# Optimization experiments

Measured on AMD Instinct MI355X. Metric: run time of the kernel, lower is better.

Reference implementation:

```python
import jax, jax.numpy as jnp
import numpy as np

B, L, IN_DIM, D_MODEL = 4, 1024, 128, 256
MDIM = 2 * D_MODEL          # mamba_dim = 512 (must equal 2*d_model for shape consistency)
NL = 4                      # mamba_layers
DIN = 2 * MDIM              # d_inner (expand=2)
NST = 16                    # d_state
DTR = MDIM // 16            # dt_rank = 32
KC = 4                      # d_conv
EPS = 1e-5

# sinusoidal positional encoding buffer (deterministic)
_pos = np.arange(L, dtype=np.float32)[:, None]
_div = np.exp(np.arange(0, MDIM, 2, dtype=np.float32) * (-np.log(10000.0) / MDIM))
_pe = np.zeros((L, MDIM), dtype=np.float32)
_pe[:, 0::2] = np.sin(_pos * _div)
_pe[:, 1::2] = np.cos(_pos * _div)
PE = jnp.asarray(_pe)


def setup_inputs() -> dict:
    key = jax.random.key(0)
    ks = iter(jax.random.split(key, 64))
    rn = lambda shape, s=0.02: jax.random.normal(next(ks), shape, jnp.float32) * s
    inp = {
        "x": jax.random.normal(next(ks), (B, L, IN_DIM), jnp.float32),
        "rtg": jax.random.normal(next(ks), (B, L, 1), jnp.float32),
        "state_emb_w": rn((D_MODEL, IN_DIM)), "state_emb_b": jnp.zeros((D_MODEL,)),
        "reward_emb_w": rn((D_MODEL, 1)), "reward_emb_b": jnp.zeros((D_MODEL,)),
        "ln_w": jnp.ones((MDIM,)), "ln_b": jnp.zeros((MDIM,)),
        "in_proj_w": rn((NL, 2 * DIN, MDIM)),
        "conv_w": rn((NL, DIN, KC), 0.1), "conv_b": jnp.zeros((NL, DIN)),
        "x_proj_w": rn((NL, DTR + 2 * NST, DIN)),
        "dt_proj_w": rn((NL, DIN, DTR), 0.1), "dt_proj_b": jnp.full((NL, DIN), -2.0),
        "A_log": jnp.tile(jnp.log(jnp.arange(1, NST + 1, dtype=jnp.float32)), (NL, DIN, 1)),
        "D_param": jnp.ones((NL, DIN)),
        "out_proj_w": rn((NL, MDIM, DIN)),
        "norm_w": jnp.ones((NL, MDIM)), "norm_f_w": jnp.ones((MDIM,)),
        "so_w1": rn((MDIM // 2, MDIM)), "so_b1": jnp.zeros((MDIM // 2,)),
        "so_w2": rn((IN_DIM, MDIM // 2)), "so_b2": jnp.zeros((IN_DIM,)),
        "ro_w1": rn((MDIM // 2, MDIM)), "ro_b1": jnp.zeros((MDIM // 2,)),
        "ro_w2": rn((1, MDIM // 2)), "ro_b2": jnp.zeros((1,)),
    }
    return inp


def _rmsnorm(h, w):
    return h * jax.lax.rsqrt(jnp.mean(h * h, -1, keepdims=True) + EPS) * w


def _mamba(h, ipw, cw, cb, xpw, dpw, dpb, Alog, Dp, opw):
    # h: [B,L,MDIM]
    Ls = h.shape[1]
    xz = h @ ipw.T                                   # [B,L,2*DIN]
    xx, z = jnp.split(xz, 2, axis=-1)
    # causal depthwise conv, kernel KC, left pad KC-1
    xp = jnp.pad(xx, ((0, 0), (KC - 1, 0), (0, 0)))
    xc = cb + sum(cw[:, k] * xp[:, k:k + Ls, :] for k in range(KC))
    xc = jax.nn.silu(xc)                             # [B,L,DIN]
    dbc = xc @ xpw.T                                 # [B,L,DTR+2*NST]
    dt = jax.nn.softplus(dbc[..., :DTR] @ dpw.T + dpb)   # [B,L,DIN]
    Bm = dbc[..., DTR:DTR + NST]                     # [B,L,NST]
    Cm = dbc[..., DTR + NST:]                        # [B,L,NST]
    A = -jnp.exp(Alog)                               # [DIN,NST]

    def step(hc, inp):
        dt_t, B_t, C_t, x_t = inp                    # [B,DIN],[B,NST],[B,NST],[B,DIN]
        hc = jnp.exp(dt_t[:, :, None] * A) * hc + (dt_t * x_t)[:, :, None] * B_t[:, None, :]
        return hc, jnp.einsum('bdn,bn->bd', hc, C_t)

    h0 = jnp.zeros((h.shape[0], DIN, NST), h.dtype)
    _, ys = jax.lax.scan(step, h0, (dt.swapaxes(0, 1), Bm.swapaxes(0, 1),
                                    Cm.swapaxes(0, 1), xc.swapaxes(0, 1)))
    y = ys.swapaxes(0, 1) + Dp * xc
    y = y * jax.nn.silu(z)
    return y @ opw.T                                 # [B,L,MDIM]


def _forward(x, rtg, state_emb_w, state_emb_b, reward_emb_w, reward_emb_b, ln_w, ln_b,
             in_proj_w, conv_w, conv_b, x_proj_w, dt_proj_w, dt_proj_b, A_log, D_param,
             out_proj_w, norm_w, norm_f_w, so_w1, so_b1, so_w2, so_b2, ro_w1, ro_b1, ro_w2, ro_b2):
    se = x @ state_emb_w.T + state_emb_b            # [B,L,D_MODEL]
    re = rtg @ reward_emb_w.T + reward_emb_b        # [B,L,D_MODEL]
    h = jnp.concatenate([se, re], axis=-1)          # [B,L,MDIM]
    h = h + PE[:h.shape[1]]                          # dropout is identity at eval
    mu = jnp.mean(h, -1, keepdims=True)
    var = jnp.var(h, -1, keepdims=True)
    h = (h - mu) * jax.lax.rsqrt(var + EPS) * ln_w + ln_b
    residual = None
    for i in range(NL):
        residual = h if residual is None else h + residual
        hn = _rmsnorm(residual, norm_w[i])
        h = _mamba(hn, in_proj_w[i], conv_w[i], conv_b[i], x_proj_w[i],
                   dt_proj_w[i], dt_proj_b[i], A_log[i], D_param[i], out_proj_w[i])
    residual = h + residual
    h = _rmsnorm(residual, norm_f_w)
    next_state = jax.nn.relu(h @ so_w1.T + so_b1) @ so_w2.T + so_b2   # [B,L,IN_DIM]
    next_reward = jax.nn.relu(h @ ro_w1.T + ro_b1) @ ro_w2.T + ro_b2  # [B,L,1]
    return next_state, next_reward


def reference(x, rtg, state_emb_w, state_emb_b, reward_emb_w, reward_emb_b, ln_w, ln_b,
              in_proj_w, conv_w, conv_b, x_proj_w, dt_proj_w, dt_proj_b, A_log, D_param,
              out_proj_w, norm_w, norm_f_w, so_w1, so_b1, so_w2, so_b2, ro_w1, ro_b1, ro_w2, ro_b2):
    return _forward(x, rtg, state_emb_w, state_emb_b, reward_emb_w, reward_emb_b, ln_w, ln_b,
                    in_proj_w, conv_w, conv_b, x_proj_w, dt_proj_w, dt_proj_b, A_log, D_param,
                    out_proj_w, norm_w, norm_f_w, so_w1, so_b1, so_w2, so_b2, ro_w1, ro_b1, ro_w2, ro_b2)
```

## Files before the change

kernel.cpp:

```cpp
#include <hip/hip_runtime.h>
#include <stdint.h>

typedef unsigned short u16;
typedef __attribute__((ext_vector_type(8))) short bf16x8;
typedef __attribute__((ext_vector_type(8))) u16 u16x8;
typedef __attribute__((ext_vector_type(4))) float f32x4;

static __device__ __forceinline__ u16 f2b(float f) {
  uint32_t u = __builtin_bit_cast(uint32_t, f);
  u += 0x7fffu + ((u >> 16) & 1u);
  return (u16)(u >> 16);
}
static __device__ __forceinline__ float b2f(u16 h) {
  uint32_t u = ((uint32_t)h) << 16;
  return __builtin_bit_cast(float, u);
}

#define GLDS16(gsrc, ldst)                                                        \
  __builtin_amdgcn_global_load_lds(                                               \
      (const __attribute__((address_space(1))) void*)(gsrc),                      \
      (__attribute__((address_space(3))) void*)(ldst), 16, 0, 0)

__global__ __launch_bounds__(256) void cvt6_kernel(
    const float* __restrict__ a0, u16* __restrict__ b0,
    const float* __restrict__ a1, u16* __restrict__ b1,
    const float* __restrict__ a2, u16* __restrict__ b2,
    const float* __restrict__ a3, u16* __restrict__ b3,
    const float* __restrict__ a4, u16* __restrict__ b4,
    const float* __restrict__ a5, u16* __restrict__ b5) {
  int i = blockIdx.x * 256 + threadIdx.x;
  const int n0 = 4194304, n1 = 262144, n2 = 2097152, n3 = 131072, n4 = 32768, n5 = 131072;
  if (i < n0) { b0[i] = f2b(a0[i]); return; } i -= n0;
  if (i < n1) { b1[i] = f2b(a1[i]); return; } i -= n1;
  if (i < n2) { b2[i] = f2b(a2[i]); return; } i -= n2;
  if (i < n3) { b3[i] = f2b(a3[i]); return; } i -= n3;
  if (i < n4) { b4[i] = f2b(a4[i]); return; } i -= n4;
  if (i < n5) { b5[i] = f2b(a5[i]); }
}

__global__ __launch_bounds__(256) void pe_kernel(float* __restrict__ PEt) {
  const int l = blockIdx.x;
  const float c = -9.210340371976184f / 512.f;
#pragma unroll
  for (int q = 0; q < 2; ++q) {
    int dd = threadIdx.x + q * 256;
    float div = expf((float)(2 * (dd >> 1)) * c);
    float v = (dd & 1) ? cosf((float)l * div) : sinf((float)l * div);
    PEt[(size_t)l * 512 + dd] = v;
  }
}

__global__ __launch_bounds__(256) void dpw_t_kernel(const float* __restrict__ dpw,
                                                    float* __restrict__ dpwT) {
  const int l = blockIdx.y;
  int idx = blockIdx.x * 256 + threadIdx.x;
  int j = idx >> 10, dd = idx & 1023;
  dpwT[(size_t)l * 32768 + idx] = dpw[(size_t)l * 32768 + (size_t)dd * 32 + j];
}

__global__ __launch_bounds__(256) void embed_ln2(
    const float* __restrict__ x, const float* __restrict__ rtg,
    const float* __restrict__ Wse, const float* __restrict__ bse,
    const float* __restrict__ Wre, const float* __restrict__ bre,
    const float* __restrict__ lnw, const float* __restrict__ lnb,
    const float* __restrict__ PEt, float* __restrict__ h) {
  const int tid = threadIdx.x;
  const int tok0 = blockIdx.x * 16;
  const int l0 = tok0 & 1023;
  __shared__ float xs[16][128];
  __shared__ float rt[16];
  __shared__ float sw[16][2][4];
  for (int i = tid; i < 16 * 128; i += 256) ((float*)xs)[i] = x[(size_t)tok0 * 128 + i];
  if (tid < 16) rt[tid] = rtg[tok0 + tid];
  __syncthreads();
  const int d = tid;
  float acc[16];
#pragma unroll
  for (int tt = 0; tt < 16; ++tt) acc[tt] = 0.f;
  const float* wrow = Wse + (size_t)d * 128;
  for (int k0 = 0; k0 < 128; k0 += 8) {
    float4 wa = *(const float4*)(wrow + k0);
    float4 wb = *(const float4*)(wrow + k0 + 4);
#pragma unroll
    for (int tt = 0; tt < 16; ++tt) {
      const float* xr = &xs[tt][k0];
      acc[tt] += xr[0] * wa.x + xr[1] * wa.y + xr[2] * wa.z + xr[3] * wa.w +
                 xr[4] * wb.x + xr[5] * wb.y + xr[6] * wb.z + xr[7] * wb.w;
    }
  }
  const float seb = bse[d], reW = Wre[d], reB = bre[d];
  const int lane = tid & 63, wv = tid >> 6;
  float h1a[16];
#pragma unroll
  for (int tt = 0; tt < 16; ++tt) {
    float h0 = acc[tt] + seb + PEt[(size_t)(l0 + tt) * 512 + d];
    float h1 = reB + rt[tt] * reW + PEt[(size_t)(l0 + tt) * 512 + 256 + d];
    acc[tt] = h0;
    h1a[tt] = h1;
    float s = h0 + h1, q = h0 * h0 + h1 * h1;
#pragma unroll
    for (int o = 32; o; o >>= 1) { s += __shfl_xor(s, o); q += __shfl_xor(q, o); }
    if (lane == 0) { sw[tt][0][wv] = s; sw[tt][1][wv] = q; }
  }
  __syncthreads();
#pragma unroll
  for (int tt = 0; tt < 16; ++tt) {
    float S = sw[tt][0][0] + sw[tt][0][1] + sw[tt][0][2] + sw[tt][0][3];
    float Q = sw[tt][1][0] + sw[tt][1][1] + sw[tt][1][2] + sw[tt][1][3];
    float mean = S * (1.f / 512.f);
    float var = Q * (1.f / 512.f) - mean * mean;
    float rstd = rsqrtf(var + 1e-5f);
    size_t base = (size_t)(tok0 + tt) * 512;
    h[base + d]       = (acc[tt] - mean) * rstd * lnw[d] + lnb[d];
    h[base + 256 + d] = (h1a[tt] - mean) * rstd * lnw[256 + d] + lnb[256 + d];
  }
}

__global__ __launch_bounds__(256) void resid_rms_kernel(
    const float* __restrict__ hin, float* __restrict__ residual,
    const float* __restrict__ w, u16* __restrict__ outb, int first) {
  const int tok = blockIdx.x;
  const int t = threadIdx.x;
  __shared__ float rq[4];
  size_t base = (size_t)tok * 512;
  float v0 = hin[base + t], v1 = hin[base + t + 256];
  if (!first) { v0 += residual[base + t]; v1 += residual[base + t + 256]; }
  residual[base + t] = v0;
  residual[base + t + 256] = v1;
  float q = v0 * v0 + v1 * v1;
#pragma unroll
  for (int o = 32; o; o >>= 1) q += __shfl_xor(q, o);
  if ((t & 63) == 0) rq[t >> 6] = q;
  __syncthreads();
  float Q = rq[0] + rq[1] + rq[2] + rq[3];
  float scale = rsqrtf(Q * (1.f / 512.f) + 1e-5f);
  outb[base + t]       = f2b(v0 * scale * w[t]);
  outb[base + t + 256] = f2b(v1 * scale * w[t + 256]);
}

template <int BM, int BN, int WM, int WN, int EPI>
__global__ __launch_bounds__(256) void gemm_bt(
    const u16* __restrict__ A, const u16* __restrict__ Bw,
    float* __restrict__ Cf, u16* __restrict__ Cb,
    const float* __restrict__ bias, int M, int N, int K) {
  constexpr int MF = BM / (WM * 16);
  constexpr int NF = BN / (WN * 16);
  constexpr int NCA = (BM * 4) / 256;
  constexpr int NCB = (BN * 4) / 256;
  __shared__ __align__(16) u16 lA[BM * 32];
  __shared__ __align__(16) u16 lB[BN * 32];
  const int tid = threadIdx.x;
  const int lane = tid & 63;
  const int wv = tid >> 6;
  const int wr = wv / WN, wc = wv % WN;
  const int m0 = blockIdx.x * BM, n0 = blockIdx.y * BN;
  const int kchunk = K / gridDim.z;
  const int kb = blockIdx.z * kchunk;

  f32x4 acc[MF][NF];
#pragma unroll
  for (int i = 0; i < MF; ++i)
#pragma unroll
    for (int j = 0; j < NF; ++j) acc[i][j] = (f32x4){0.f, 0.f, 0.f, 0.f};

  const int srow = tid >> 2, sck = tid & 3;
  const u16* Ag = A + (size_t)(m0 + srow) * K + sck * 8 + kb;
  const u16* Bg = Bw + (size_t)(n0 + srow) * K + sck * 8 + kb;

  for (int k0 = 0; k0 < kchunk; k0 += 32) {
#pragma unroll
    for (int it = 0; it < NCA; ++it)
      GLDS16(Ag + (size_t)it * 64 * K + k0, &lA[(it * 256 + tid) * 8]);
#pragma unroll
    for (int it = 0; it < NCB; ++it)
      GLDS16(Bg + (size_t)it * 64 * K + k0, &lB[(it * 256 + tid) * 8]);
    __syncthreads();
    bf16x8 af[MF], bfr[NF];
    const int koff = (lane >> 4) * 8;
#pragma unroll
    for (int mi = 0; mi < MF; ++mi) {
      int r = wr * (MF * 16) + mi * 16 + (lane & 15);
      af[mi] = *(const bf16x8*)(&lA[r * 32 + koff]);
    }
#pragma unroll
    for (int ni = 0; ni < NF; ++ni) {
      int r = wc * (NF * 16) + ni * 16 + (lane & 15);
      bfr[ni] = *(const bf16x8*)(&lB[r * 32 + koff]);
    }
#pragma unroll
    for (int mi = 0; mi < MF; ++mi)
#pragma unroll
      for (int ni = 0; ni < NF; ++ni)
        acc[mi][ni] = __builtin_amdgcn_mfma_f32_16x16x32_bf16(af[mi], bfr[ni], acc[mi][ni], 0, 0, 0);
    __syncthreads();
  }

  float* co = Cf + (size_t)blockIdx.z * (size_t)M * N;
  const int rbase = (lane >> 4) * 4;
  const int cbase = lane & 15;
#pragma unroll
  for (int mi = 0; mi < MF; ++mi) {
#pragma unroll
    for (int ni = 0; ni < NF; ++ni) {
      int row = m0 + wr * (MF * 16) + mi * 16 + rbase;
      int col = n0 + wc * (NF * 16) + ni * 16 + cbase;
      float bv = (EPI >= 2) ? bias[col] : 0.f;
#pragma unroll
      for (int r = 0; r < 4; ++r) {
        float v = acc[mi][ni][r] + bv;
        if (EPI == 2) v = fmaxf(v, 0.f);
        size_t idx = (size_t)(row + r) * N + col;
        if (EPI == 1 || EPI == 2) Cb[idx] = f2b(v);
        else co[idx] = v;
      }
    }
  }
}

__global__ __launch_bounds__(256) void conv_silu_kernel2(
    const u16* __restrict__ xz, const float* __restrict__ cw,
    const float* __restrict__ cb, u16* __restrict__ xcb) {
  int gid = blockIdx.x * 256 + threadIdx.x;
  int d0 = (gid & 127) * 8;
  int token = gid >> 7;
  int t = token & 1023;
  const u16* xx = xz + (size_t)(token - t) * 2048 + d0;
  float s[8];
#pragma unroll
  for (int j = 0; j < 8; ++j) s[j] = cb[d0 + j];
#pragma unroll
  for (int k = 0; k < 4; ++k) {
    int tt = t - 3 + k;
    if (tt >= 0) {
      u16x8 v = *(const u16x8*)(xx + (size_t)tt * 2048);
#pragma unroll
      for (int j = 0; j < 8; ++j) s[j] += cw[(size_t)(d0 + j) * 4 + k] * b2f(v[j]);
    }
  }
  u16x8 o;
#pragma unroll
  for (int j = 0; j < 8; ++j) {
    float sl = s[j] / (1.f + expf(-s[j]));
    o[j] = f2b(sl);
  }
  *(u16x8*)(xcb + (size_t)token * 1024 + d0) = o;
}

__global__ __launch_bounds__(256) void dt_kernel2(
    const float* __restrict__ P, const float* __restrict__ dpwT,
    const float* __restrict__ dpb, u16* __restrict__ dtout,
    float* __restrict__ dbcr) {
  const int tid = threadIdx.x;
  const int tok0 = blockIdx.x * 16;
  __shared__ float sm[16][64];
  const size_t str = (size_t)4096 * 64;
  for (int i = tid; i < 16 * 64; i += 256) {
    size_t o = (size_t)tok0 * 64 + i;
    float v = P[o] + P[str + o] + P[2 * str + o] + P[3 * str + o];
    ((float*)sm)[i] = v;
    dbcr[o] = v;
  }
  __syncthreads();
  float acc0[16], acc1[16], acc2[16], acc3[16];
#pragma unroll
  for (int t = 0; t < 16; ++t) { acc0[t] = 0.f; acc1[t] = 0.f; acc2[t] = 0.f; acc3[t] = 0.f; }
#pragma unroll 4
  for (int j = 0; j < 32; ++j) {
    float w0 = dpwT[(size_t)j * 1024 + tid];
    float w1 = dpwT[(size_t)j * 1024 + 256 + tid];
    float w2 = dpwT[(size_t)j * 1024 + 512 + tid];
    float w3 = dpwT[(size_t)j * 1024 + 768 + tid];
#pragma unroll
    for (int t = 0; t < 16; ++t) {
      float sv = sm[t][j];
      acc0[t] += sv * w0;
      acc1[t] += sv * w1;
      acc2[t] += sv * w2;
      acc3[t] += sv * w3;
    }
  }
  const float b0 = dpb[tid], b1 = dpb[256 + tid], b2 = dpb[512 + tid], b3 = dpb[768 + tid];
#pragma unroll
  for (int t = 0; t < 16; ++t) {
    size_t o = (size_t)(tok0 + t) * 1024 + tid;
    float a0 = acc0[t] + b0, a1 = acc1[t] + b1, a2 = acc2[t] + b2, a3 = acc3[t] + b3;
    dtout[o]       = f2b((a0 > 20.f) ? a0 : logf(1.f + expf(a0)));
    dtout[o + 256] = f2b((a1 > 20.f) ? a1 : logf(1.f + expf(a1)));
    dtout[o + 512] = f2b((a2 > 20.f) ? a2 : logf(1.f + expf(a2)));
    dtout[o + 768] = f2b((a3 > 20.f) ? a3 : logf(1.f + expf(a3)));
  }
}

__global__ __launch_bounds__(256) void scan1(
    const u16* __restrict__ dt, const u16* __restrict__ xc,
    const float* __restrict__ dbc, const float* __restrict__ Alog,
    float* __restrict__ Ubuf, float* __restrict__ SD, int NCc, int TCc) {
  const int d = blockIdx.x * 256 + threadIdx.x;
  const int c = blockIdx.y;
  const int b = blockIdx.z;
  const int t0 = c * TCc;
  __shared__ __align__(16) float sB[64][16];
  for (int i = threadIdx.x; i < TCc * 16; i += 256) {
    int t = i >> 4, n = i & 15;
    sB[t][n] = dbc[((size_t)(b * 1024 + t0 + t)) * 64 + 32 + n];
  }
  float A2[16];
#pragma unroll
  for (int q = 0; q < 4; ++q) {
    float4 a4 = *(const float4*)(Alog + (size_t)d * 16 + q * 4);
    A2[q * 4 + 0] = -expf(a4.x) * 1.4426950408889634f;
    A2[q * 4 + 1] = -expf(a4.y) * 1.4426950408889634f;
    A2[q * 4 + 2] = -expf(a4.z) * 1.4426950408889634f;
    A2[q * 4 + 3] = -expf(a4.w) * 1.4426950408889634f;
  }
  __syncthreads();
  float hc[16];
#pragma unroll
  for (int n = 0; n < 16; ++n) hc[n] = 0.f;
  float sumdt = 0.f;
  size_t tok = (size_t)b * 1024 + t0;
  for (int t = 0; t < TCc; ++t, ++tok) {
    float dtv = b2f(dt[tok * 1024 + d]);
    float xcv = b2f(xc[tok * 1024 + d]);
    float du = dtv * xcv;
    sumdt += dtv;
#pragma unroll
    for (int q = 0; q < 4; ++q) {
      float4 B4 = *(const float4*)(&sB[t][q * 4]);
      float e0 = exp2f(dtv * A2[q * 4 + 0]);
      float e1 = exp2f(dtv * A2[q * 4 + 1]);
      float e2 = exp2f(dtv * A2[q * 4 + 2]);
      float e3 = exp2f(dtv * A2[q * 4 + 3]);
      hc[q * 4 + 0] = e0 * hc[q * 4 + 0] + du * B4.x;
      hc[q * 4 + 1] = e1 * hc[q * 4 + 1] + du * B4.y;
      hc[q * 4 + 2] = e2 * hc[q * 4 + 2] + du * B4.z;
      hc[q * 4 + 3] = e3 * hc[q * 4 + 3] + du * B4.w;
    }
  }
  size_t ob = (((size_t)b * NCc + c) * 16) * 1024 + d;
#pragma unroll
  for (int n = 0; n < 16; ++n) Ubuf[ob + (size_t)n * 1024] = hc[n];
  SD[((size_t)b * NCc + c) * 1024 + d] = sumdt;
}

__global__ __launch_bounds__(256) void scan_mid(
    const float* __restrict__ Ubuf, const float* __restrict__ SD,
    const float* __restrict__ Alog, float* __restrict__ H0, int NCc) {
  int idx = blockIdx.x * 256 + threadIdx.x;
  int b = idx >> 14;
  int nd = idx & 16383;
  int n = nd >> 10, d = nd & 1023;
  const float A2 = -expf(Alog[(size_t)d * 16 + n]) * 1.4426950408889634f;
  float h = 0.f;
  size_t o0 = ((size_t)b * NCc * 16) * 1024 + nd;
  const size_t cstr = (size_t)16 * 1024;
  size_t sd0 = ((size_t)b * NCc) * 1024 + d;
  for (int cc = 0; cc < NCc; ++cc) {
    size_t o = o0 + (size_t)cc * cstr;
    H0[o] = h;
    if (cc < NCc - 1) {
      float e = exp2f(A2 * SD[sd0 + (size_t)cc * 1024]);
      h = e * h + Ubuf[o];
    }
  }
}

__global__ __launch_bounds__(256) void scan2(
    const u16* __restrict__ dt, const u16* __restrict__ xc,
    const float* __restrict__ dbc, const u16* __restrict__ xz,
    const float* __restrict__ Alog, const float* __restrict__ Dp,
    const float* __restrict__ H0, u16* __restrict__ yg, int NCc, int TCc) {
  const int d = blockIdx.x * 256 + threadIdx.x;
  const int c = blockIdx.y;
  const int b = blockIdx.z;
  const int t0 = c * TCc;
  __shared__ __align__(16) float sB[64][16];
  __shared__ __align__(16) float sC[64][16];
  for (int i = threadIdx.x; i < TCc * 16; i += 256) {
    int t = i >> 4, n = i & 15;
    size_t o = ((size_t)(b * 1024 + t0 + t)) * 64 + 32;
    sB[t][n] = dbc[o + n];
    sC[t][n] = dbc[o + 16 + n];
  }
  float A2[16];
#pragma unroll
  for (int q = 0; q < 4; ++q) {
    float4 a4 = *(const float4*)(Alog + (size_t)d * 16 + q * 4);
    A2[q * 4 + 0] = -expf(a4.x) * 1.4426950408889634f;
    A2[q * 4 + 1] = -expf(a4.y) * 1.4426950408889634f;
    A2[q * 4 + 2] = -expf(a4.z) * 1.4426950408889634f;
    A2[q * 4 + 3] = -expf(a4.w) * 1.4426950408889634f;
  }
  const float Dd = Dp[d];
  float hc[16];
  size_t ob = (((size_t)b * NCc + c) * 16) * 1024 + d;
#pragma unroll
  for (int n = 0; n < 16; ++n) hc[n] = H0[ob + (size_t)n * 1024];
  __syncthreads();
  size_t tok = (size_t)b * 1024 + t0;
  for (int t = 0; t < TCc; ++t, ++tok) {
    float dtv = b2f(dt[tok * 1024 + d]);
    float xcv = b2f(xc[tok * 1024 + d]);
    float du = dtv * xcv;
    float y0 = 0.f, y1 = 0.f, y2 = 0.f, y3 = 0.f;
#pragma unroll
    for (int q = 0; q < 4; ++q) {
      float4 B4 = *(const float4*)(&sB[t][q * 4]);
      float4 C4 = *(const float4*)(&sC[t][q * 4]);
      float e0 = exp2f(dtv * A2[q * 4 + 0]);
      float e1 = exp2f(dtv * A2[q * 4 + 1]);
      float e2 = exp2f(dtv * A2[q * 4 + 2]);
      float e3 = exp2f(dtv * A2[q * 4 + 3]);
      hc[q * 4 + 0] = e0 * hc[q * 4 + 0] + du * B4.x;
      hc[q * 4 + 1] = e1 * hc[q * 4 + 1] + du * B4.y;
      hc[q * 4 + 2] = e2 * hc[q * 4 + 2] + du * B4.z;
      hc[q * 4 + 3] = e3 * hc[q * 4 + 3] + du * B4.w;
      y0 += hc[q * 4 + 0] * C4.x;
      y1 += hc[q * 4 + 1] * C4.y;
      y2 += hc[q * 4 + 2] * C4.z;
      y3 += hc[q * 4 + 3] * C4.w;
    }
    float y = (y0 + y1) + (y2 + y3);
    float z = b2f(xz[tok * 2048 + 1024 + d]);
    float g = z / (1.f + expf(-z));
    yg[tok * 1024 + d] = f2b((y + Dd * xcv) * g);
  }
}

__global__ __launch_bounds__(256) void reward_head_kernel(
    const u16* __restrict__ t1r, const float* __restrict__ w2,
    const float* __restrict__ b2, float* __restrict__ outr) {
  int tok = blockIdx.x * 4 + (threadIdx.x >> 6);
  int lane = threadIdx.x & 63;
  float s = 0.f;
#pragma unroll
  for (int j = 0; j < 256; j += 64) s += b2f(t1r[(size_t)tok * 256 + j + lane]) * w2[j + lane];
#pragma unroll
  for (int o = 32; o; o >>= 1) s += __shfl_xor(s, o);
  if (lane == 0) outr[tok] = s + b2[0];
}

extern "C" void kernel_launch(void* const* d_in, const int* in_sizes, int n_in,
                              void* d_out, int out_size, void* d_ws, size_t ws_size,
                              hipStream_t stream) {
  const float* x    = (const float*)d_in[0];
  const float* rtg  = (const float*)d_in[1];
  const float* Wse  = (const float*)d_in[2];
  const float* bse  = (const float*)d_in[3];
  const float* Wre  = (const float*)d_in[4];
  const float* bre  = (const float*)d_in[5];
  const float* lnw  = (const float*)d_in[6];
  const float* lnb  = (const float*)d_in[7];
  const float* ipw  = (const float*)d_in[8];
  const float* cw   = (const float*)d_in[9];
  const float* cb   = (const float*)d_in[10];
  const float* xpw  = (const float*)d_in[11];
  const float* dpw  = (const float*)d_in[12];
  const float* dpb  = (const float*)d_in[13];
  const float* Alog = (const float*)d_in[14];
  const float* Dp   = (const float*)d_in[15];
  const float* opw  = (const float*)d_in[16];
  const float* nw   = (const float*)d_in[17];
  const float* nfw  = (const float*)d_in[18];
  const float* sow1 = (const float*)d_in[19];
  const float* sob1 = (const float*)d_in[20];
  const float* sow2 = (const float*)d_in[21];
  const float* sob2 = (const float*)d_in[22];
  const float* row1 = (const float*)d_in[23];
  const float* rob1 = (const float*)d_in[24];
  const float* row2 = (const float*)d_in[25];
  const float* rob2 = (const float*)d_in[26];
  (void)in_sizes; (void)n_in; (void)out_size;

  char* wsp = (char*)d_ws;
  size_t off = 0;
  auto alloc = [&](size_t bytes) -> void* {
    off = (off + 255) & ~(size_t)255;
    void* p = wsp + off;
    off += bytes;
    return p;
  };
  const int TOK = 4096;
  float* h     = (float*)alloc((size_t)TOK * 512 * 4);
  float* resid = (float*)alloc((size_t)TOK * 512 * 4);
  u16* hn      = (u16*)alloc((size_t)TOK * 512 * 2);
  u16* xzb     = (u16*)alloc((size_t)TOK * 2048 * 2);
  u16* xcb     = (u16*)alloc((size_t)TOK * 1024 * 2);
  float* dbcP  = (float*)alloc((size_t)4 * TOK * 64 * 4);
  float* dbc   = (float*)alloc((size_t)TOK * 64 * 4);
  u16* dtb     = (u16*)alloc((size_t)TOK * 1024 * 2);
  float* PEt   = (float*)alloc((size_t)1024 * 512 * 4);
  float* dpwT  = (float*)alloc((size_t)4 * 32 * 1024 * 4);
  u16* ipwb    = (u16*)alloc((size_t)4 * 2048 * 512 * 2);
  u16* xpwb    = (u16*)alloc((size_t)4 * 64 * 1024 * 2);
  u16* opwb    = (u16*)alloc((size_t)4 * 512 * 1024 * 2);
  u16* sow1b   = (u16*)alloc((size_t)256 * 512 * 2);
  u16* sow2b   = (u16*)alloc((size_t)128 * 256 * 2);
  u16* row1b   = (u16*)alloc((size_t)256 * 512 * 2);

  size_t base_off = (off + 255) & ~(size_t)255;
  auto scan_bytes = [](int nc) {
    return (size_t)2 * 4 * nc * 16 * 1024 * 4 + (size_t)4 * nc * 1024 * 4 + 1024;
  };
  int NCc = 16;
  if (ws_size >= base_off + scan_bytes(64)) NCc = 64;
  else if (ws_size >= base_off + scan_bytes(32)) NCc = 32;
  int TCc = 1024 / NCc;
  char* shared8 = (char*)alloc((size_t)4096 * NCc * 16 * 4);
  float* Ubuf  = (float*)shared8;
  float* H0    = (float*)alloc((size_t)4096 * NCc * 16 * 4);
  float* SD    = (float*)alloc((size_t)4 * NCc * 1024 * 4);
  u16* t1s     = (u16*)shared8;
  u16* t1r     = t1s + (size_t)TOK * 256;

  cvt6_kernel<<<26752, 256, 0, stream>>>(ipw, ipwb, xpw, xpwb, opw, opwb,
                                         sow1, sow1b, sow2, sow2b, row1, row1b);
  pe_kernel<<<1024, 256, 0, stream>>>(PEt);
  dpw_t_kernel<<<dim3(128, 4), 256, 0, stream>>>(dpw, dpwT);
  embed_ln2<<<256, 256, 0, stream>>>(x, rtg, Wse, bse, Wre, bre, lnw, lnb, PEt, h);

  for (int i = 0; i < 4; ++i) {
    resid_rms_kernel<<<TOK, 256, 0, stream>>>(h, resid, nw + i * 512, hn, i == 0);
    gemm_bt<128, 128, 2, 2, 1><<<dim3(32, 16, 1), 256, 0, stream>>>(
        hn, ipwb + (size_t)i * 2048 * 512, nullptr, xzb, nullptr, 4096, 2048, 512);
    conv_silu_kernel2<<<2048, 256, 0, stream>>>(
        xzb, cw + (size_t)i * 4096, cb + i * 1024, xcb);
    gemm_bt<128, 64, 2, 2, 0><<<dim3(32, 1, 4), 256, 0, stream>>>(
        xcb, xpwb + (size_t)i * 64 * 1024, dbcP, nullptr, nullptr, 4096, 64, 1024);
    dt_kernel2<<<TOK / 16, 256, 0, stream>>>(dbcP, dpwT + (size_t)i * 32 * 1024,
                                             dpb + i * 1024, dtb, dbc);
    scan1<<<dim3(4, NCc - 1, 4), 256, 0, stream>>>(
        dtb, xcb, dbc, Alog + (size_t)i * 1024 * 16, Ubuf, SD, NCc, TCc);
    scan_mid<<<256, 256, 0, stream>>>(Ubuf, SD, Alog + (size_t)i * 1024 * 16, H0, NCc);
    scan2<<<dim3(4, NCc, 4), 256, 0, stream>>>(
        dtb, xcb, dbc, xzb, Alog + (size_t)i * 1024 * 16, Dp + i * 1024,
        H0, xcb, NCc, TCc);
    gemm_bt<128, 64, 2, 2, 0><<<dim3(32, 8, 1), 256, 0, stream>>>(
        xcb, opwb + (size_t)i * 512 * 1024, h, nullptr, nullptr, 4096, 512, 1024);
  }

  resid_rms_kernel<<<TOK, 256, 0, stream>>>(h, resid, nfw, hn, 0);
  gemm_bt<64, 64, 2, 2, 2><<<dim3(64, 4, 1), 256, 0, stream>>>(
      hn, sow1b, nullptr, t1s, sob1, 4096, 256, 512);
  gemm_bt<64, 64, 2, 2, 3><<<dim3(64, 2, 1), 256, 0, stream>>>(
      t1s, sow2b, (float*)d_out, nullptr, sob2, 4096, 128, 256);
  gemm_bt<64, 64, 2, 2, 2><<<dim3(64, 4, 1), 256, 0, stream>>>(
      hn, row1b, nullptr, t1r, rob1, 4096, 256, 512);
  reward_head_kernel<<<TOK / 4, 256, 0, stream>>>(
      t1r, row2, rob2, (float*)d_out + (size_t)TOK * 128);
}
```

Before: 776.9 us.

## Fuse scan into one cooperative kernel, merge setup kernels and head GEMMs

```diff
diff --git a/kernel.cpp b/kernel.cpp
--- a/kernel.cpp
+++ b/kernel.cpp
@@ -1,5 +1,8 @@
 #include <hip/hip_runtime.h>
+#include <hip/hip_cooperative_groups.h>
 #include <stdint.h>
+
+namespace cg = cooperative_groups;
 
 typedef unsigned short u16;
 typedef __attribute__((ext_vector_type(8))) short bf16x8;
@@ -21,41 +24,39 @@
       (const __attribute__((address_space(1))) void*)(gsrc),                      \
       (__attribute__((address_space(3))) void*)(ldst), 16, 0, 0)
 
-__global__ __launch_bounds__(256) void cvt6_kernel(
-    const float* __restrict__ a0, u16* __restrict__ b0,
-    const float* __restrict__ a1, u16* __restrict__ b1,
-    const float* __restrict__ a2, u16* __restrict__ b2,
-    const float* __restrict__ a3, u16* __restrict__ b3,
-    const float* __restrict__ a4, u16* __restrict__ b4,
-    const float* __restrict__ a5, u16* __restrict__ b5) {
+__global__ __launch_bounds__(256) void setup_kernel(
+    const float* __restrict__ ipw, u16* __restrict__ ipwb,
+    const float* __restrict__ xpw, u16* __restrict__ xpwb,
+    const float* __restrict__ opw, u16* __restrict__ opwb,
+    const float* __restrict__ sow1, u16* __restrict__ sow1b,
+    const float* __restrict__ sow2, u16* __restrict__ sow2b,
+    const float* __restrict__ row1, u16* __restrict__ row1b,
+    float* __restrict__ PEt,
+    const float* __restrict__ dpw, float* __restrict__ dpwT,
+    const float* __restrict__ cw, float* __restrict__ cwT) {
   int i = blockIdx.x * 256 + threadIdx.x;
-  const int n0 = 4194304, n1 = 262144, n2 = 2097152, n3 = 131072, n4 = 32768, n5 = 131072;
-  if (i < n0) { b0[i] = f2b(a0[i]); return; } i -= n0;
-  if (i < n1) { b1[i] = f2b(a1[i]); return; } i -= n1;
-  if (i < n2) { b2[i] = f2b(a2[i]); return; } i -= n2;
-  if (i < n3) { b3[i] = f2b(a3[i]); return; } i -= n3;
-  if (i < n4) { b4[i] = f2b(a4[i]); return; } i -= n4;
-  if (i < n5) { b5[i] = f2b(a5[i]); }
-}
-
-__global__ __launch_bounds__(256) void pe_kernel(float* __restrict__ PEt) {
-  const int l = blockIdx.x;
-  const float c = -9.210340371976184f / 512.f;
-#pragma unroll
-  for (int q = 0; q < 2; ++q) {
-    int dd = threadIdx.x + q * 256;
-    float div = expf((float)(2 * (dd >> 1)) * c);
-    float v = (dd & 1) ? cosf((float)l * div) : sinf((float)l * div);
-    PEt[(size_t)l * 512 + dd] = v;
-  }
-}
-
-__global__ __launch_bounds__(256) void dpw_t_kernel(const float* __restrict__ dpw,
-                                                    float* __restrict__ dpwT) {
-  const int l = blockIdx.y;
-  int idx = blockIdx.x * 256 + threadIdx.x;
-  int j = idx >> 10, dd = idx & 1023;
-  dpwT[(size_t)l * 32768 + idx] = dpw[(size_t)l * 32768 + (size_t)dd * 32 + j];
+  if (i < 4194304) { ipwb[i] = f2b(ipw[i]); return; } i -= 4194304;
+  if (i < 262144)  { xpwb[i] = f2b(xpw[i]); return; } i -= 262144;
+  if (i < 2097152) { opwb[i] = f2b(opw[i]); return; } i -= 2097152;
+  if (i < 131072)  { sow1b[i] = f2b(sow1[i]); return; } i -= 131072;
+  if (i < 32768)   { sow2b[i] = f2b(sow2[i]); return; } i -= 32768;
+  if (i < 131072)  { row1b[i] = f2b(row1[i]); return; } i -= 131072;
+  if (i < 524288) {
+    int dd = i & 511, l = i >> 9;
+    const float cc = -9.210340371976184f / 512.f;
+    float div = expf((float)(2 * (dd >> 1)) * cc);
+    PEt[i] = (dd & 1) ? cosf((float)l * div) : sinf((float)l * div);
+    return;
+  } i -= 524288;
+  if (i < 131072) {
+    int l = i >> 15, r = i & 32767, j = r >> 10, dd = r & 1023;
+    dpwT[i] = dpw[(size_t)l * 32768 + (size_t)dd * 32 + j];
+    return;
+  } i -= 131072;
+  if (i < 16384) {
+    int l = i >> 12, r = i & 4095, k = r >> 10, dd = r & 1023;
+    cwT[i] = cw[(size_t)l * 4096 + (size_t)dd * 4 + k];
+  }
 }
 
 __global__ __launch_bounds__(256) void embed_ln2(
@@ -142,7 +143,8 @@
 __global__ __launch_bounds__(256) void gemm_bt(
     const u16* __restrict__ A, const u16* __restrict__ Bw,
     float* __restrict__ Cf, u16* __restrict__ Cb,
-    const float* __restrict__ bias, int M, int N, int K) {
+    const float* __restrict__ bias, const float* __restrict__ bias2,
+    int M, int N, int K, int As) {
   constexpr int MF = BM / (WM * 16);
   constexpr int NF = BN / (WN * 16);
   constexpr int NCA = (BM * 4) / 256;
@@ -164,13 +166,13 @@
     for (int j = 0; j < NF; ++j) acc[i][j] = (f32x4){0.f, 0.f, 0.f, 0.f};
 
   const int srow = tid >> 2, sck = tid & 3;
-  const u16* Ag = A + (size_t)(m0 + srow) * K + sck * 8 + kb;
+  const u16* Ag = A + (size_t)(m0 + srow) * As + sck * 8 + kb;
   const u16* Bg = Bw + (size_t)(n0 + srow) * K + sck * 8 + kb;
 
   for (int k0 = 0; k0 < kchunk; k0 += 32) {
 #pragma unroll
     for (int it = 0; it < NCA; ++it)
-      GLDS16(Ag + (size_t)it * 64 * K + k0, &lA[(it * 256 + tid) * 8]);
+      GLDS16(Ag + (size_t)it * 64 * As + k0, &lA[(it * 256 + tid) * 8]);
 #pragma unroll
     for (int it = 0; it < NCB; ++it)
       GLDS16(Bg + (size_t)it * 64 * K + k0, &lB[(it * 256 + tid) * 8]);
@@ -204,21 +206,23 @@
     for (int ni = 0; ni < NF; ++ni) {
       int row = m0 + wr * (MF * 16) + mi * 16 + rbase;
       int col = n0 + wc * (NF * 16) + ni * 16 + cbase;
-      float bv = (EPI >= 2) ? bias[col] : 0.f;
+      float bv = 0.f;
+      if (EPI == 2 || EPI == 3) bv = bias[col];
+      if (EPI == 4) bv = (col < 256) ? bias[col] : bias2[col - 256];
 #pragma unroll
       for (int r = 0; r < 4; ++r) {
         float v = acc[mi][ni][r] + bv;
-        if (EPI == 2) v = fmaxf(v, 0.f);
+        if (EPI == 2 || EPI == 4) v = fmaxf(v, 0.f);
         size_t idx = (size_t)(row + r) * N + col;
-        if (EPI == 1 || EPI == 2) Cb[idx] = f2b(v);
+        if (EPI == 1 || EPI == 2 || EPI == 4) Cb[idx] = f2b(v);
         else co[idx] = v;
       }
     }
   }
 }
 
-__global__ __launch_bounds__(256) void conv_silu_kernel2(
-    const u16* __restrict__ xz, const float* __restrict__ cw,
+__global__ __launch_bounds__(256) void conv_silu3(
+    const u16* __restrict__ xz, const float* __restrict__ cwT,
     const float* __restrict__ cb, u16* __restrict__ xcb) {
   int gid = blockIdx.x * 256 + threadIdx.x;
   int d0 = (gid & 127) * 8;
@@ -226,15 +230,23 @@
   int t = token & 1023;
   const u16* xx = xz + (size_t)(token - t) * 2048 + d0;
   float s[8];
-#pragma unroll
-  for (int j = 0; j < 8; ++j) s[j] = cb[d0 + j];
+  {
+    float4 cba = *(const float4*)(cb + d0);
+    float4 cbb = *(const float4*)(cb + d0 + 4);
+    s[0] = cba.x; s[1] = cba.y; s[2] = cba.z; s[3] = cba.w;
+    s[4] = cbb.x; s[5] = cbb.y; s[6] = cbb.z; s[7] = cbb.w;
+  }
 #pragma unroll
   for (int k = 0; k < 4; ++k) {
     int tt = t - 3 + k;
     if (tt >= 0) {
       u16x8 v = *(const u16x8*)(xx + (size_t)tt * 2048);
-#pragma unroll
-      for (int j = 0; j < 8; ++j) s[j] += cw[(size_t)(d0 + j) * 4 + k] * b2f(v[j]);
+      float4 wA = *(const float4*)(cwT + (size_t)k * 1024 + d0);
+      float4 wB = *(const float4*)(cwT + (size_t)k * 1024 + d0 + 4);
+      s[0] += wA.x * b2f(v[0]); s[1] += wA.y * b2f(v[1]);
+      s[2] += wA.z * b2f(v[2]); s[3] += wA.w * b2f(v[3]);
+      s[4] += wB.x * b2f(v[4]); s[5] += wB.y * b2f(v[5]);
+      s[6] += wB.z * b2f(v[6]); s[7] += wB.w * b2f(v[7]);
     }
   }
   u16x8 o;
@@ -291,18 +303,28 @@
   }
 }
 
-__global__ __launch_bounds__(256) void scan1(
+#define NCF 32
+#define TCF 32
+
+__global__ __launch_bounds__(256, 2) void scanF(
     const u16* __restrict__ dt, const u16* __restrict__ xc,
-    const float* __restrict__ dbc, const float* __restrict__ Alog,
-    float* __restrict__ Ubuf, float* __restrict__ SD, int NCc, int TCc) {
-  const int d = blockIdx.x * 256 + threadIdx.x;
+    const float* __restrict__ dbc, const u16* __restrict__ xz,
+    const float* __restrict__ Alog, const float* __restrict__ Dp,
+    float* __restrict__ Ubuf, float* __restrict__ SD,
+    u16* __restrict__ yg) {
+  const int tid = threadIdx.x;
+  const int d = blockIdx.x * 256 + tid;
   const int c = blockIdx.y;
   const int b = blockIdx.z;
-  const int t0 = c * TCc;
-  __shared__ __align__(16) float sB[64][16];
-  for (int i = threadIdx.x; i < TCc * 16; i += 256) {
+  const int t0 = c * TCF;
+  __shared__ __align__(16) float sB[TCF][16];
+  __shared__ __align__(16) float sC[TCF][16];
+  __shared__ float sYL[TCF][256];
+  for (int i = tid; i < TCF * 16; i += 256) {
     int t = i >> 4, n = i & 15;
-    sB[t][n] = dbc[((size_t)(b * 1024 + t0 + t)) * 64 + 32 + n];
+    size_t o = ((size_t)(b * 1024 + t0 + t)) * 64 + 32;
+    sB[t][n] = dbc[o + n];
+    sC[t][n] = dbc[o + 16 + n];
   }
   float A2[16];
 #pragma unroll
@@ -313,95 +335,21 @@
     A2[q * 4 + 2] = -expf(a4.z) * 1.4426950408889634f;
     A2[q * 4 + 3] = -expf(a4.w) * 1.4426950408889634f;
   }
+  const float Dd = Dp[d];
   __syncthreads();
   float hc[16];
 #pragma unroll
   for (int n = 0; n < 16; ++n) hc[n] = 0.f;
+  float cd[TCF];
   float sumdt = 0.f;
   size_t tok = (size_t)b * 1024 + t0;
-  for (int t = 0; t < TCc; ++t, ++tok) {
+#pragma unroll
+  for (int t = 0; t < TCF; ++t, ++tok) {
     float dtv = b2f(dt[tok * 1024 + d]);
     float xcv = b2f(xc[tok * 1024 + d]);
     float du = dtv * xcv;
     sumdt += dtv;
-#pragma unroll
-    for (int q = 0; q < 4; ++q) {
-      float4 B4 = *(const float4*)(&sB[t][q * 4]);
-      float e0 = exp2f(dtv * A2[q * 4 + 0]);
-      float e1 = exp2f(dtv * A2[q * 4 + 1]);
-      float e2 = exp2f(dtv * A2[q * 4 + 2]);
-      float e3 = exp2f(dtv * A2[q * 4 + 3]);
-      hc[q * 4 + 0] = e0 * hc[q * 4 + 0] + du * B4.x;
-      hc[q * 4 + 1] = e1 * hc[q * 4 + 1] + du * B4.y;
-      hc[q * 4 + 2] = e2 * hc[q * 4 + 2] + du * B4.z;
-      hc[q * 4 + 3] = e3 * hc[q * 4 + 3] + du * B4.w;
-    }
-  }
-  size_t ob = (((size_t)b * NCc + c) * 16) * 1024 + d;
-#pragma unroll
-  for (int n = 0; n < 16; ++n) Ubuf[ob + (size_t)n * 1024] = hc[n];
-  SD[((size_t)b * NCc + c) * 1024 + d] = sumdt;
-}
-
-__global__ __launch_bounds__(256) void scan_mid(
-    const float* __restrict__ Ubuf, const float* __restrict__ SD,
-    const float* __restrict__ Alog, float* __restrict__ H0, int NCc) {
-  int idx = blockIdx.x * 256 + threadIdx.x;
-  int b = idx >> 14;
-  int nd = idx & 16383;
-  int n = nd >> 10, d = nd & 1023;
-  const float A2 = -expf(Alog[(size_t)d * 16 + n]) * 1.4426950408889634f;
-  float h = 0.f;
-  size_t o0 = ((size_t)b * NCc * 16) * 1024 + nd;
-  const size_t cstr = (size_t)16 * 1024;
-  size_t sd0 = ((size_t)b * NCc) * 1024 + d;
-  for (int cc = 0; cc < NCc; ++cc) {
-    size_t o = o0 + (size_t)cc * cstr;
-    H0[o] = h;
-    if (cc < NCc - 1) {
-      float e = exp2f(A2 * SD[sd0 + (size_t)cc * 1024]);
-      h = e * h + Ubuf[o];
-    }
-  }
-}
-
-__global__ __launch_bounds__(256) void scan2(
-    const u16* __restrict__ dt, const u16* __restrict__ xc,
-    const float* __restrict__ dbc, const u16* __restrict__ xz,
-    const float* __restrict__ Alog, const float* __restrict__ Dp,
-    const float* __restrict__ H0, u16* __restrict__ yg, int NCc, int TCc) {
-  const int d = blockIdx.x * 256 + threadIdx.x;
-  const int c = blockIdx.y;
-  const int b = blockIdx.z;
-  const int t0 = c * TCc;
-  __shared__ __align__(16) float sB[64][16];
-  __shared__ __align__(16) float sC[64][16];
-  for (int i = threadIdx.x; i < TCc * 16; i += 256) {
-    int t = i >> 4, n = i & 15;
-    size_t o = ((size_t)(b * 1024 + t0 + t)) * 64 + 32;
-    sB[t][n] = dbc[o + n];
-    sC[t][n] = dbc[o + 16 + n];
-  }
-  float A2[16];
-#pragma unroll
-  for (int q = 0; q < 4; ++q) {
-    float4 a4 = *(const float4*)(Alog + (size_t)d * 16 + q * 4);
-    A2[q * 4 + 0] = -expf(a4.x) * 1.4426950408889634f;
-    A2[q * 4 + 1] = -expf(a4.y) * 1.4426950408889634f;
-    A2[q * 4 + 2] = -expf(a4.z) * 1.4426950408889634f;
-    A2[q * 4 + 3] = -expf(a4.w) * 1.4426950408889634f;
-  }
-  const float Dd = Dp[d];
-  float hc[16];
-  size_t ob = (((size_t)b * NCc + c) * 16) * 1024 + d;
-#pragma unroll
-  for (int n = 0; n < 16; ++n) hc[n] = H0[ob + (size_t)n * 1024];
-  __syncthreads();
-  size_t tok = (size_t)b * 1024 + t0;
-  for (int t = 0; t < TCc; ++t, ++tok) {
-    float dtv = b2f(dt[tok * 1024 + d]);
-    float xcv = b2f(xc[tok * 1024 + d]);
-    float du = dtv * xcv;
+    cd[t] = sumdt;
     float y0 = 0.f, y1 = 0.f, y2 = 0.f, y3 = 0.f;
 #pragma unroll
     for (int q = 0; q < 4; ++q) {
@@ -420,21 +368,63 @@
       y2 += hc[q * 4 + 2] * C4.z;
       y3 += hc[q * 4 + 3] * C4.w;
     }
-    float y = (y0 + y1) + (y2 + y3);
+    sYL[t][tid] = (y0 + y1) + (y2 + y3) + Dd * xcv;
+  }
+  size_t ob = (((size_t)b * NCF + c) * 16) * 1024 + d;
+#pragma unroll
+  for (int n = 0; n < 16; ++n) Ubuf[ob + (size_t)n * 1024] = hc[n];
+  SD[((size_t)b * NCF + c) * 1024 + d] = sumdt;
+
+  cg::this_grid().sync();
+
+  tok = (size_t)b * 1024 + t0;
+  if (c == 0) {
+#pragma unroll
+    for (int t = 0; t < TCF; ++t, ++tok) {
+      float acc = sYL[t][tid];
+      float z = b2f(xz[tok * 2048 + 1024 + d]);
+      float g = z / (1.f + expf(-z));
+      yg[tok * 1024 + d] = f2b(acc * g);
+    }
+    return;
+  }
+  float h0[16];
+#pragma unroll
+  for (int n = 0; n < 16; ++n) h0[n] = 0.f;
+  for (int ccp = 0; ccp < c; ++ccp) {
+    float sd = SD[((size_t)b * NCF + ccp) * 1024 + d];
+    size_t oo = (((size_t)b * NCF + ccp) * 16) * 1024 + d;
+#pragma unroll
+    for (int n = 0; n < 16; ++n)
+      h0[n] = exp2f(A2[n] * sd) * h0[n] + Ubuf[oo + (size_t)n * 1024];
+  }
+#pragma unroll
+  for (int t = 0; t < TCF; ++t, ++tok) {
+    float acc = sYL[t][tid];
+    float cdt = cd[t];
+#pragma unroll
+    for (int q = 0; q < 4; ++q) {
+      float4 C4 = *(const float4*)(&sC[t][q * 4]);
+      acc += C4.x * exp2f(A2[q * 4 + 0] * cdt) * h0[q * 4 + 0];
+      acc += C4.y * exp2f(A2[q * 4 + 1] * cdt) * h0[q * 4 + 1];
+      acc += C4.z * exp2f(A2[q * 4 + 2] * cdt) * h0[q * 4 + 2];
+      acc += C4.w * exp2f(A2[q * 4 + 3] * cdt) * h0[q * 4 + 3];
+    }
     float z = b2f(xz[tok * 2048 + 1024 + d]);
     float g = z / (1.f + expf(-z));
-    yg[tok * 1024 + d] = f2b((y + Dd * xcv) * g);
+    yg[tok * 1024 + d] = f2b(acc * g);
   }
 }
 
 __global__ __launch_bounds__(256) void reward_head_kernel(
-    const u16* __restrict__ t1r, const float* __restrict__ w2,
+    const u16* __restrict__ t1sr, const float* __restrict__ w2,
     const float* __restrict__ b2, float* __restrict__ outr) {
   int tok = blockIdx.x * 4 + (threadIdx.x >> 6);
   int lane = threadIdx.x & 63;
   float s = 0.f;
 #pragma unroll
-  for (int j = 0; j < 256; j += 64) s += b2f(t1r[(size_t)tok * 256 + j + lane]) * w2[j + lane];
+  for (int j = 0; j < 256; j += 64)
+    s += b2f(t1sr[(size_t)tok * 512 + 256 + j + lane]) * w2[j + lane];
 #pragma unroll
   for (int o = 32; o; o >>= 1) s += __shfl_xor(s, o);
   if (lane == 0) outr[tok] = s + b2[0];
@@ -470,7 +460,7 @@
   const float* rob1 = (const float*)d_in[24];
   const float* row2 = (const float*)d_in[25];
   const float* rob2 = (const float*)d_in[26];
-  (void)in_sizes; (void)n_in; (void)out_size;
+  (void)in_sizes; (void)n_in; (void)out_size; (void)ws_size;
 
   char* wsp = (char*)d_ws;
   size_t off = 0;
@@ -491,61 +481,58 @@
   u16* dtb     = (u16*)alloc((size_t)TOK * 1024 * 2);
   float* PEt   = (float*)alloc((size_t)1024 * 512 * 4);
   float* dpwT  = (float*)alloc((size_t)4 * 32 * 1024 * 4);
+  float* cwT   = (float*)alloc((size_t)4 * 4 * 1024 * 4);
   u16* ipwb    = (u16*)alloc((size_t)4 * 2048 * 512 * 2);
   u16* xpwb    = (u16*)alloc((size_t)4 * 64 * 1024 * 2);
   u16* opwb    = (u16*)alloc((size_t)4 * 512 * 1024 * 2);
   u16* sow1b   = (u16*)alloc((size_t)256 * 512 * 2);
+  u16* row1b   = (u16*)alloc((size_t)256 * 512 * 2);
   u16* sow2b   = (u16*)alloc((size_t)128 * 256 * 2);
-  u16* row1b   = (u16*)alloc((size_t)256 * 512 * 2);
-
-  size_t base_off = (off + 255) & ~(size_t)255;
-  auto scan_bytes = [](int nc) {
-    return (size_t)2 * 4 * nc * 16 * 1024 * 4 + (size_t)4 * nc * 1024 * 4 + 1024;
-  };
-  int NCc = 16;
-  if (ws_size >= base_off + scan_bytes(64)) NCc = 64;
-  else if (ws_size >= base_off + scan_bytes(32)) NCc = 32;
-  int TCc = 1024 / NCc;
-  char* shared8 = (char*)alloc((size_t)4096 * NCc * 16 * 4);
-  float* Ubuf  = (float*)shared8;
-  float* H0    = (float*)alloc((size_t)4096 * NCc * 16 * 4);
-  float* SD    = (float*)alloc((size_t)4 * NCc * 1024 * 4);
-  u16* t1s     = (u16*)shared8;
-  u16* t1r     = t1s + (size_t)TOK * 256;
-
-  cvt6_kernel<<<26752, 256, 0, stream>>>(ipw, ipwb, xpw, xpwb, opw, opwb,
-                                         sow1, sow1b, sow2, sow2b, row1, row1b);
-  pe_kernel<<<1024, 256, 0, stream>>>(PEt);
-  dpw_t_kernel<<<dim3(128, 4), 256, 0, stream>>>(dpw, dpwT);
+  float* Ubuf  = (float*)alloc((size_t)4096 * NCF * 16 * 4);
+  float* SD    = (float*)alloc((size_t)4 * NCF * 1024 * 4);
+  u16* t1sr    = (u16*)Ubuf;
+
+  setup_kernel<<<29376, 256, 0, stream>>>(ipw, ipwb, xpw, xpwb, opw, opwb,
+                                          sow1, sow1b, sow2, sow2b, row1, row1b,
+                                          PEt, dpw, dpwT, cw, cwT);
   embed_ln2<<<256, 256, 0, stream>>>(x, rtg, Wse, bse, Wre, bre, lnw, lnb, PEt, h);
 
   for (int i = 0; i < 4; ++i) {
     resid_rms_kernel<<<TOK, 256, 0, stream>>>(h, resid, nw + i * 512, hn, i == 0);
     gemm_bt<128, 128, 2, 2, 1><<<dim3(32, 16, 1), 256, 0, stream>>>(
-        hn, ipwb + (size_t)i * 2048 * 512, nullptr, xzb, nullptr, 4096, 2048, 512);
-    conv_silu_kernel2<<<2048, 256, 0, stream>>>(
-        xzb, cw + (size_t)i * 4096, cb + i * 1024, xcb);
+        hn, ipwb + (size_t)i * 2048 * 512, nullptr, xzb, nullptr, nullptr,
+        4096, 2048, 512, 512);
+    conv_silu3<<<2048, 256, 0, stream>>>(
+        xzb, cwT + (size_t)i * 4096, cb + i * 1024, xcb);
     gemm_bt<128, 64, 2, 2, 0><<<dim3(32, 1, 4), 256, 0, stream>>>(
-        xcb, xpwb + (size_t)i * 64 * 1024, dbcP, nullptr, nullptr, 4096, 64, 1024);
+        xcb, xpwb + (size_t)i * 64 * 1024, dbcP, nullptr, nullptr, nullptr,
+        4096, 64, 1024, 1024);
     dt_kernel2<<<TOK / 16, 256, 0, stream>>>(dbcP, dpwT + (size_t)i * 32 * 1024,
                                              dpb + i * 1024, dtb, dbc);
-    scan1<<<dim3(4, NCc - 1, 4), 256, 0, stream>>>(
-        dtb, xcb, dbc, Alog + (size_t)i * 1024 * 16, Ubuf, SD, NCc, TCc);
-    scan_mid<<<256, 256, 0, stream>>>(Ubuf, SD, Alog + (size_t)i * 1024 * 16, H0, NCc);
-    scan2<<<dim3(4, NCc, 4), 256, 0, stream>>>(
-        dtb, xcb, dbc, xzb, Alog + (size_t)i * 1024 * 16, Dp + i * 1024,
-        H0, xcb, NCc, TCc);
+    {
+      const u16* dtp = dtb;
+      const u16* xcp = xcb;
+      const float* dbcp = dbc;
+      const u16* xzp = xzb;
+      const float* AlogL = Alog + (size_t)i * 1024 * 16;
+      const float* DpL = Dp + (size_t)i * 1024;
+      float* Up = Ubuf;
+      float* SDp = SD;
+      u16* ygp = xcb;
+      void* sargs[] = {&dtp, &xcp, &dbcp, &xzp, &AlogL, &DpL, &Up, &SDp, &ygp};
+      hipLaunchCooperativeKernel((void*)scanF, dim3(4, NCF, 4), dim3(256, 1, 1),
+                                 sargs, 0, stream);
+    }
     gemm_bt<128, 64, 2, 2, 0><<<dim3(32, 8, 1), 256, 0, stream>>>(
-        xcb, opwb + (size_t)i * 512 * 1024, h, nullptr, nullptr, 4096, 512, 1024);
+        xcb, opwb + (size_t)i * 512 * 1024, h, nullptr, nullptr, nullptr,
+        4096, 512, 1024, 1024);
   }
 
   resid_rms_kernel<<<TOK, 256, 0, stream>>>(h, resid, nfw, hn, 0);
-  gemm_bt<64, 64, 2, 2, 2><<<dim3(64, 4, 1), 256, 0, stream>>>(
-      hn, sow1b, nullptr, t1s, sob1, 4096, 256, 512);
+  gemm_bt<64, 64, 2, 2, 4><<<dim3(64, 8, 1), 256, 0, stream>>>(
+      hn, sow1b, nullptr, t1sr, sob1, rob1, 4096, 512, 512, 512);
   gemm_bt<64, 64, 2, 2, 3><<<dim3(64, 2, 1), 256, 0, stream>>>(
-      t1s, sow2b, (float*)d_out, nullptr, sob2, 4096, 128, 256);
-  gemm_bt<64, 64, 2, 2, 2><<<dim3(64, 4, 1), 256, 0, stream>>>(
-      hn, row1b, nullptr, t1r, rob1, 4096, 256, 512);
+      t1sr, sow2b, (float*)d_out, nullptr, sob2, nullptr, 4096, 128, 256, 512);
   reward_head_kernel<<<TOK / 4, 256, 0, stream>>>(
-      t1r, row2, rob2, (float*)d_out + (size_t)TOK * 128);
-}
+      t1sr, row2, rob2, (float*)d_out + (size_t)TOK * 128);
+}
```

Result: slower. 902.0 us (+16.1%).
